# Optimization experiments

Measured on AMD Instinct MI355X. Metric: run time of the kernel, lower is better.

The kernel has to match this reference:

```python
import jax, jax.numpy as jnp
import numpy as np

JITTER = 0.05  # posterior-covariance jitter (constructor arg `jitter`)
TWO_PI = 2.0 * np.pi


def _local_k(x1, x2, ls, std):
    # 1-D RBF kernel: x1 (A,), x2 (B,) -> (A, B)
    d2 = jnp.square(x1[:, None] - x2[None, :])
    return (std * std) * jnp.exp(-0.5 * d2 / (ls * ls))


def setup_inputs() -> dict:
    key = jax.random.key(0)
    ks = jax.random.split(key, 8)
    N, D, M = 3072, 4, 512
    X = jax.random.normal(ks[0], (N, D), dtype=jnp.float32)
    y = jax.random.normal(ks[1], (N, 1), dtype=jnp.float32)
    X_bar = jax.random.normal(ks[2], (M, D), dtype=jnp.float32)
    # learned parameters (moderate positive values so fp32 Choleskys are stable)
    local_gp_ls = 1.0 + 0.1 * jax.random.normal(ks[3], (D,), dtype=jnp.float32)
    local_gp_std = 0.5 + 0.05 * jax.random.normal(ks[4], (D,), dtype=jnp.float32)
    local_gp_noise_std = 0.3 * jnp.ones((D,), dtype=jnp.float32)
    local_ls = 0.3 + 0.5 * jax.random.uniform(ks[5], (M, D), dtype=jnp.float32)
    global_gp_std = jnp.array([0.7], dtype=jnp.float32)
    global_gp_noise_std = jnp.array([0.5], dtype=jnp.float32)
    return {
        "X": X, "y": y, "X_bar": X_bar,
        "local_gp_ls": local_gp_ls, "local_gp_std": local_gp_std,
        "local_gp_noise_std": local_gp_noise_std, "local_ls": local_ls,
        "global_gp_std": global_gp_std, "global_gp_noise_std": global_gp_noise_std,
    }


def reference(X, y, X_bar, local_gp_ls, local_gp_std, local_gp_noise_std,
              local_ls, global_gp_std, global_gp_noise_std):
    # NSGP.nlml() in training mode.
    N, D = X.shape
    M = X_bar.shape[0]
    dtype = X.dtype
    eyeM = jnp.eye(M, dtype=dtype)
    eyeN = jnp.eye(N, dtype=dtype)
    log_lbar = jnp.log(jnp.abs(local_ls))  # (M, D)

    def per_dim(xb, xd, ls, std, noise, loglb):
        # local GP over inducing points for one input dimension
        k = _local_k(xb, xb, ls, std) + (noise * noise) * eyeM  # (M, M)
        c = jnp.linalg.cholesky(k)
        alpha = jax.scipy.linalg.cho_solve((c, True), loglb[:, None])  # (M, 1)
        kstar = _local_k(xd, xb, ls, std)  # (N, M)
        l = jnp.exp(kstar @ alpha)[:, 0]   # (N,) predicted lengthscales
        kss = _local_k(xd, xd, ls, std)    # (N, N)
        v = jax.scipy.linalg.cho_solve((c, True), kstar.T)  # (M, N)
        kpost = kss - kstar @ v + JITTER * eyeN             # posterior cov
        pc = jnp.linalg.cholesky(kpost)
        Bd = jnp.sum(jnp.log(jnp.diagonal(pc)))
        return l, Bd

    # batch the per-dimension local-GP work across the D input dims
    l_dn, B_d = jax.vmap(per_dim, in_axes=(1, 1, 0, 0, 0, 1))(
        X_bar, X, local_gp_ls, local_gp_std, local_gp_noise_std, log_lbar)
    l = l_dn.T  # (N, D)

    # nonstationary global kernel (Gibbs kernel)
    l1 = l[:, None, :]                    # (N, 1, D)
    l2 = l[None, :, :]                    # (1, N, D)
    lsq = l1 * l1 + l2 * l2               # (N, N, D)
    suffix = jnp.prod(jnp.sqrt(2.0 * l1 * l2 / lsq), axis=2)  # (N, N)
    d2 = jnp.square(X[:, None, :] - X[None, :, :])            # (N, N, D)
    gvar = global_gp_std[0] * global_gp_std[0]
    K = gvar * suffix * jnp.exp(-jnp.sum(d2 / lsq, axis=2))
    K = K + (global_gp_noise_std[0] ** 2) * eyeN

    L = jnp.linalg.cholesky(K)
    alpha = jax.scipy.linalg.cho_solve((L, True), y)  # (N, 1)
    log2pi = jnp.log(jnp.asarray(TWO_PI, dtype))
    A = 0.5 * ((y.T @ alpha)[0, 0]
               + jnp.sum(jnp.log(jnp.diagonal(L)))
               + N * log2pi)
    B = jnp.sum(B_d) + 0.5 * (M * D * log2pi)
    return A + B
```

## Files before the change

kernel.cpp:

```cpp
#include <hip/hip_runtime.h>
#include <math.h>

#define N_   3072
#define D_   4
#define M_   512
#define NPAD 3200
#define NB   128
#define PW   32
#define NBLK (NPAD/NB)
#define MBLK (M_/NB)
#define JITTER_ 0.05f
#define CBORD 32768.0f

__global__ __launch_bounds__(256)
void k_potrf_inv(float* Abase, size_t aStride, int lda, int kblk,
                 float* TinvBase, size_t tStride, int doInv,
                 float* logsum, int slotBase, int limit) {
  __shared__ float LT[NB*NB];
  __shared__ float Wp[10*PW*PW];
  __shared__ float Tt[3*PW*PW];
  __shared__ float pivd[NB];
  const int tid = threadIdx.x;
  float* A = Abase + (size_t)blockIdx.z * aStride;
  const int j0 = kblk * NB;

  for (int t = tid; t < NB*NB; t += 256) {
    int r = t & 127, c = t >> 7;
    LT[c*NB + r] = (c <= r) ? A[(size_t)(j0 + r)*lda + (j0 + c)] : 0.f;
  }
  __syncthreads();

  #pragma unroll
  for (int p = 0; p < 4; ++p) {
    const int pc0 = p*PW, pc1 = pc0 + PW;
    for (int j = pc0; j < pc1; ++j) {
      float d = fmaxf(LT[j*NB + j], 1e-30f);
      if (tid == 0) pivd[j] = d;
      float rd = 1.0f / d;
      int w = pc1 - 1 - j;
      for (int t = tid; t < w*NB; t += 256) {
        int c = j + 1 + (t >> 7);
        int i = t & 127;
        if (i >= c)
          LT[c*NB + i] -= LT[j*NB + i] * LT[j*NB + c] * rd;
      }
      __syncthreads();
    }
    for (int t = tid; t < PW*NB; t += 256) {
      int jc = pc0 + (t >> 7);
      int i  = t & 127;
      float dd = pivd[jc];
      if (i > jc)       LT[jc*NB + i] *= rsqrtf(dd);
      else if (i == jc) LT[jc*NB + i] = sqrtf(dd);
    }
    __syncthreads();
    if (pc1 < NB) {
      const int rem = NB - pc1;
      for (int t = tid; t < rem*rem; t += 256) {
        int cc = t / rem, rr = t - cc*rem;
        int c = pc1 + cc, i = pc1 + rr;
        if (i >= c) {
          float s = 0.f;
          #pragma unroll
          for (int jj = 0; jj < PW; ++jj)
            s += LT[(pc0+jj)*NB + i] * LT[(pc0+jj)*NB + c];
          LT[c*NB + i] -= s;
        }
      }
      __syncthreads();
    }
  }

  for (int t = tid; t < NB*NB; t += 256) {
    int r = t & 127, c = t >> 7;
    if (c <= r) A[(size_t)(j0 + r)*lda + (j0 + c)] = LT[c*NB + r];
  }
  {
    float lg = 0.f;
    if (tid < NB) {
      int g = j0 + tid;
      if (g < limit) lg = 0.5f * logf(pivd[tid]);
    }
    for (int o = 32; o; o >>= 1) lg += __shfl_down(lg, o);
    int wv = tid >> 6;
    if ((tid & 63) == 0 && wv < 2)
      logsum[(slotBase + blockIdx.z*32 + kblk)*2 + wv] = lg;
  }

  if (!doInv) return;

  for (int t = tid; t < 4*1024; t += 256) {
    int I = t >> 10, e = t & 1023;
    int r = e >> 5, c = e & 31;
    Wp[(I*(I+1)/2 + I)*1024 + e] = (r == c) ? 1.f : 0.f;
  }
  __syncthreads();
  {
    int wI = tid >> 6;
    int lane = tid & 63;
    float* Rb = &Wp[(wI*(wI+1)/2 + wI)*1024];
    for (int j = 0; j < 32; ++j) {
      float dinv = 1.0f / LT[(wI*32+j)*NB + (wI*32+j)];
      for (int t = lane; t < 1024; t += 64) {
        int i = t >> 5, c = t & 31;
        if (i > j && c <= j)
          Rb[i*32 + c] -= LT[(wI*32+j)*NB + (wI*32+i)] * Rb[j*32 + c] * dinv;
      }
      __syncthreads();
    }
    for (int t = lane; t < 1024; t += 64) {
      int i = t >> 5, c = t & 31;
      if (c <= i) Rb[t] *= 1.0f / LT[(wI*32+i)*NB + (wI*32+i)];
    }
    __syncthreads();
  }
  #pragma unroll
  for (int dist = 1; dist < 4; ++dist) {
    const int nb = 4 - dist;
    for (int t = tid; t < nb*1024; t += 256) {
      int b = t >> 10, e = t & 1023;
      int r = e >> 5, c = e & 31;
      int J = b, I = b + dist;
      float s = 0.f;
      for (int K = J; K < I; ++K) {
        const float* Wkj = &Wp[(K*(K+1)/2 + J)*1024];
        #pragma unroll
        for (int k = 0; k < 32; ++k)
          s += LT[(K*32+k)*NB + (I*32+r)] * Wkj[k*32 + c];
      }
      Tt[b*1024 + e] = s;
    }
    __syncthreads();
    for (int t = tid; t < nb*1024; t += 256) {
      int b = t >> 10, e = t & 1023;
      int r = e >> 5, c = e & 31;
      int J = b, I = b + dist;
      const float* Wii = &Wp[(I*(I+1)/2 + I)*1024];
      float s = 0.f;
      #pragma unroll
      for (int k = 0; k < 32; ++k)
        s += Wii[r*32 + k] * Tt[b*1024 + k*32 + c];
      Wp[(I*(I+1)/2 + J)*1024 + e] = -s;
    }
    __syncthreads();
  }
  {
    float* Tinv = TinvBase + (size_t)blockIdx.z * tStride;
    for (int t = tid; t < NB*32; t += 256) {
      int i = t >> 5, c4 = (t & 31) * 4;
      int I = i >> 5, J = c4 >> 5;
      float4 v;
      if (J <= I) {
        const float* Wij = &Wp[(I*(I+1)/2 + J)*1024 + (i & 31)*32 + (c4 & 31)];
        v = *(const float4*)Wij;
      } else v = make_float4(0.f, 0.f, 0.f, 0.f);
      *(float4*)&Tinv[i*NB + c4] = v;
    }
  }
}

__global__ __launch_bounds__(256)
void k_trsm(float* Abase, size_t aStride, int lda, int kblk,
            const float* TinvBase, size_t tStride) {
  __shared__ float As[32*68];
  __shared__ float Ts[32*132];
  const int tid = threadIdx.x;
  float* A = Abase + (size_t)blockIdx.z * aStride;
  const float* Tinv = TinvBase + (size_t)blockIdx.z * tStride;
  const int k0 = kblk * NB;
  const int row0 = k0 + NB + blockIdx.x * 64;
  const int tx = tid & 15, ty = tid >> 4;
  float acc[4][8];
  #pragma unroll
  for (int i = 0; i < 4; ++i)
    #pragma unroll
    for (int u = 0; u < 8; ++u) acc[i][u] = 0.f;
  for (int ks = 0; ks < NB; ks += 32) {
    for (int t = tid; t < 64*8; t += 256) {
      int r = t >> 3, q = t & 7;
      float4 v = *(const float4*)&A[(size_t)(row0 + r)*lda + k0 + ks + q*4];
      As[(q*4+0)*68 + r] = v.x; As[(q*4+1)*68 + r] = v.y;
      As[(q*4+2)*68 + r] = v.z; As[(q*4+3)*68 + r] = v.w;
    }
    for (int t = tid; t < 128*8; t += 256) {
      int c = t >> 3, q = t & 7;
      float4 v = *(const float4*)&Tinv[c*NB + ks + q*4];
      Ts[(q*4+0)*132 + c] = v.x; Ts[(q*4+1)*132 + c] = v.y;
      Ts[(q*4+2)*132 + c] = v.z; Ts[(q*4+3)*132 + c] = v.w;
    }
    __syncthreads();
    #pragma unroll
    for (int kk = 0; kk < 32; ++kk) {
      float a[4], b[8];
      *(float4*)a      = *(const float4*)&As[kk*68 + ty*4];
      *(float4*)&b[0]  = *(const float4*)&Ts[kk*132 + tx*8];
      *(float4*)&b[4]  = *(const float4*)&Ts[kk*132 + tx*8 + 4];
      #pragma unroll
      for (int i = 0; i < 4; ++i)
        #pragma unroll
        for (int u = 0; u < 8; ++u) acc[i][u] += a[i]*b[u];
    }
    __syncthreads();
  }
  #pragma unroll
  for (int i = 0; i < 4; ++i) {
    int r = row0 + ty*4 + i;
    *(float4*)&A[(size_t)r*lda + k0 + tx*8]     = make_float4(acc[i][0],acc[i][1],acc[i][2],acc[i][3]);
    *(float4*)&A[(size_t)r*lda + k0 + tx*8 + 4] = make_float4(acc[i][4],acc[i][5],acc[i][6],acc[i][7]);
  }
}

__global__ __launch_bounds__(256)
void k_syrk(float* Abase, size_t aStride, int lda, int kblk) {
  if (blockIdx.y > blockIdx.x) return;
  __shared__ float As[32*68];
  __shared__ float Bs[32*68];
  const int tid = threadIdx.x;
  float* A = Abase + (size_t)blockIdx.z * aStride;
  const int k0 = kblk * NB;
  const int row0 = k0 + NB + blockIdx.x * 64;
  const int col0 = k0 + NB + blockIdx.y * 64;
  const int tx = tid & 15, ty = tid >> 4;
  float acc[4][4];
  #pragma unroll
  for (int i=0;i<4;++i) { acc[i][0]=0.f;acc[i][1]=0.f;acc[i][2]=0.f;acc[i][3]=0.f; }
  for (int ks = 0; ks < NB; ks += 32) {
    for (int t = tid; t < 64*8; t += 256) {
      int r = t >> 3, q = t & 7;
      float4 v = *(const float4*)&A[(size_t)(row0 + r)*lda + k0 + ks + q*4];
      As[(q*4+0)*68 + r] = v.x; As[(q*4+1)*68 + r] = v.y;
      As[(q*4+2)*68 + r] = v.z; As[(q*4+3)*68 + r] = v.w;
      float4 w = *(const float4*)&A[(size_t)(col0 + r)*lda + k0 + ks + q*4];
      Bs[(q*4+0)*68 + r] = w.x; Bs[(q*4+1)*68 + r] = w.y;
      Bs[(q*4+2)*68 + r] = w.z; Bs[(q*4+3)*68 + r] = w.w;
    }
    __syncthreads();
    #pragma unroll
    for (int kk = 0; kk < 32; ++kk) {
      float a[4], b[4];
      *(float4*)a = *(const float4*)&As[kk*68 + ty*4];
      *(float4*)b = *(const float4*)&Bs[kk*68 + tx*4];
      #pragma unroll
      for (int i=0;i<4;++i)
        #pragma unroll
        for (int u=0;u<4;++u) acc[i][u] += a[i]*b[u];
    }
    __syncthreads();
  }
  #pragma unroll
  for (int i=0;i<4;++i) {
    size_t off = (size_t)(row0 + ty*4 + i)*lda + col0 + tx*4;
    float4 v = *(const float4*)&A[off];
    v.x -= acc[i][0]; v.y -= acc[i][1]; v.z -= acc[i][2]; v.w -= acc[i][3];
    *(float4*)&A[off] = v;
  }
}

__global__ __launch_bounds__(256)
void k_build_kb(const float* Xbar, const float* lsp, const float* stdp, const float* noisep,
                float* KbBase, size_t kbStride, int dimBase) {
  int z = blockIdx.z, d = dimBase + z;
  float* Kb = KbBase + (size_t)z*kbStride;
  int idx = blockIdx.x*256 + threadIdx.x;
  if (idx >= M_*M_) return;
  int i = idx >> 9, j = idx & 511;
  float ls = lsp[d], sd = stdp[d], nz = noisep[d];
  float df = Xbar[i*D_ + d] - Xbar[j*D_ + d];
  float v = sd*sd*expf(-0.5f*df*df/(ls*ls));
  if (i == j) v += nz*nz;
  Kb[idx] = v;
}

__global__ __launch_bounds__(256)
void k_build_kstar(const float* X, const float* Xbar, const float* lsp, const float* stdp,
                   float* KSBase, size_t ksStride, int dimBase) {
  int z = blockIdx.z, d = dimBase + z;
  float* KS = KSBase + (size_t)z*ksStride;
  int idx = blockIdx.x*256 + threadIdx.x;
  if (idx >= N_*M_) return;
  int i = idx >> 9, j = idx & 511;
  float ls = lsp[d], sd = stdp[d];
  float df = X[i*D_ + d] - Xbar[j*D_ + d];
  KS[idx] = sd*sd*expf(-0.5f*df*df/(ls*ls));
}

__global__ __launch_bounds__(256)
void k_csolve(float* CBase, size_t cStride, const float* KbBase, size_t kbStride,
              const float* TinvKbBase, size_t tkbStride, int J) {
  __shared__ float sm[12672];
  const int tid = threadIdx.x;
  float* C = CBase + (size_t)blockIdx.z*cStride;
  const float* L = KbBase + (size_t)blockIdx.z*kbStride;
  const float* Tinv = TinvKbBase + (size_t)blockIdx.z*tkbStride + (size_t)J*NB*NB;
  const int row0 = blockIdx.x*64;
  const int tx = tid & 15, ty = tid >> 4;
  float* As = sm; float* Ls = sm + 2176;
  float* Xs = sm; float* Ts = sm + 8448;
  float acc[4][8];
  #pragma unroll
  for (int i=0;i<4;++i) {
    const float* p = &C[(size_t)(row0+ty*4+i)*M_ + J*NB + tx*8];
    float4 v0 = *(const float4*)p, v1 = *(const float4*)(p+4);
    acc[i][0]=v0.x; acc[i][1]=v0.y; acc[i][2]=v0.z; acc[i][3]=v0.w;
    acc[i][4]=v1.x; acc[i][5]=v1.y; acc[i][6]=v1.z; acc[i][7]=v1.w;
  }
  for (int P = 0; P < J; ++P) {
    for (int ks = 0; ks < NB; ks += 32) {
      __syncthreads();
      for (int t = tid; t < 64*8; t += 256) {
        int r = t >> 3, q = t & 7;
        float4 v = *(const float4*)&C[(size_t)(row0+r)*M_ + P*NB + ks + q*4];
        As[(q*4+0)*68+r]=v.x; As[(q*4+1)*68+r]=v.y; As[(q*4+2)*68+r]=v.z; As[(q*4+3)*68+r]=v.w;
      }
      for (int t = tid; t < 128*8; t += 256) {
        int c = t >> 3, q = t & 7;
        float4 v = *(const float4*)&L[(size_t)(J*NB+c)*M_ + P*NB + ks + q*4];
        Ls[(q*4+0)*132+c]=v.x; Ls[(q*4+1)*132+c]=v.y; Ls[(q*4+2)*132+c]=v.z; Ls[(q*4+3)*132+c]=v.w;
      }
      __syncthreads();
      #pragma unroll
      for (int kk = 0; kk < 32; ++kk) {
        float a[4], b[8];
        *(float4*)a     = *(const float4*)&As[kk*68 + ty*4];
        *(float4*)&b[0] = *(const float4*)&Ls[kk*132 + tx*8];
        *(float4*)&b[4] = *(const float4*)&Ls[kk*132 + tx*8 + 4];
        #pragma unroll
        for (int i=0;i<4;++i)
          #pragma unroll
          for (int u=0;u<8;++u) acc[i][u] -= a[i]*b[u];
      }
    }
  }
  __syncthreads();
  #pragma unroll
  for (int i=0;i<4;++i)
    #pragma unroll
    for (int u=0;u<8;++u) Xs[(ty*4+i)*132 + tx*8+u] = acc[i][u];
  #pragma unroll
  for (int i=0;i<4;++i)
    #pragma unroll
    for (int u=0;u<8;++u) acc[i][u] = 0.f;
  for (int ms = 0; ms < NB; ms += 32) {
    for (int t = tid; t < 128*8; t += 256) {
      int c = t >> 3, q = t & 7;
      float4 v = *(const float4*)&Tinv[c*NB + ms + q*4];
      Ts[(q*4+0)*132+c]=v.x; Ts[(q*4+1)*132+c]=v.y; Ts[(q*4+2)*132+c]=v.z; Ts[(q*4+3)*132+c]=v.w;
    }
    __syncthreads();
    #pragma unroll
    for (int mm = 0; mm < 32; ++mm) {
      float a[4], b[8];
      a[0]=Xs[(ty*4+0)*132+ms+mm]; a[1]=Xs[(ty*4+1)*132+ms+mm];
      a[2]=Xs[(ty*4+2)*132+ms+mm]; a[3]=Xs[(ty*4+3)*132+ms+mm];
      *(float4*)&b[0] = *(const float4*)&Ts[mm*132 + tx*8];
      *(float4*)&b[4] = *(const float4*)&Ts[mm*132 + tx*8 + 4];
      #pragma unroll
      for (int i=0;i<4;++i)
        #pragma unroll
        for (int u=0;u<8;++u) acc[i][u] += a[i]*b[u];
    }
    __syncthreads();
  }
  #pragma unroll
  for (int i=0;i<4;++i) {
    float* p = &C[(size_t)(row0+ty*4+i)*M_ + J*NB + tx*8];
    *(float4*)p     = make_float4(acc[i][0],acc[i][1],acc[i][2],acc[i][3]);
    *(float4*)(p+4) = make_float4(acc[i][4],acc[i][5],acc[i][6],acc[i][7]);
  }
}

__global__ __launch_bounds__(256)
void k_fwdsub(const float* KbBase, size_t kbStride,
              const float* TkbBase, size_t tkbStride,
              const float* lls, float* wBase, size_t wStride, int dimBase) {
  __shared__ float w[M_];
  __shared__ float tv[NB];
  __shared__ float red[256];
  int z = blockIdx.z, d = dimBase + z;
  const float* L = KbBase + (size_t)z*kbStride;
  const float* Tk = TkbBase + (size_t)z*tkbStride;
  float* wout = wBase + (size_t)z*wStride;
  const int tid = threadIdx.x;
  for (int i = tid; i < M_; i += 256) w[i] = logf(fabsf(lls[i*D_ + d]));
  __syncthreads();
  const int r = tid >> 1, h = tid & 1;
  for (int J = 0; J < 4; ++J) {
    float s = 0.f;
    int half = (J*NB) >> 1;
    for (int k = h*half; k < (h+1)*half; k += 4) {
      float4 lv = *(const float4*)&L[(size_t)(J*NB + r)*M_ + k];
      s += lv.x*w[k] + lv.y*w[k+1] + lv.z*w[k+2] + lv.w*w[k+3];
    }
    red[tid] = s;
    __syncthreads();
    if (h == 0) tv[r] = w[J*NB + r] - red[2*r] - red[2*r+1];
    __syncthreads();
    const float* Ti = Tk + (size_t)J*NB*NB;
    s = 0.f;
    for (int k = h*64; k < h*64 + 64; k += 4) {
      float4 tw = *(const float4*)&Ti[r*NB + k];
      s += tw.x*tv[k] + tw.y*tv[k+1] + tw.z*tv[k+2] + tw.w*tv[k+3];
    }
    red[tid] = s;
    __syncthreads();
    if (h == 0) w[J*NB + r] = red[2*r] + red[2*r+1];
    __syncthreads();
  }
  for (int i = tid; i < M_; i += 256) wout[i] = w[i];
}

__global__ __launch_bounds__(256)
void k_gemv_l(const float* CBase, size_t cStride, const float* wBase, size_t wStride,
              float* lvec, int dimBase) {
  int z = blockIdx.z, d = dimBase + z;
  const float* C = CBase + (size_t)z*cStride;
  const float* w = wBase + (size_t)z*wStride;
  __shared__ float ws[M_];
  for (int i = threadIdx.x; i < M_; i += 256) ws[i] = w[i];
  __syncthreads();
  int wid = threadIdx.x >> 6, lane = threadIdx.x & 63;
  int row = blockIdx.x*4 + wid;
  if (row >= N_) return;
  float s = 0.f;
  const float* cr = &C[(size_t)row*M_];
  for (int k = lane; k < M_; k += 64) s += cr[k]*ws[k];
  for (int o = 32; o; o >>= 1) s += __shfl_down(s, o);
  if (lane == 0) lvec[row*D_ + d] = expf(s);
}

__global__ __launch_bounds__(256)
void k_kpost(const float* X, const float* lsp, const float* stdp,
             const float* CBase, size_t cStride,
             float* Abase, size_t aStride, int dimBase) {
  if (blockIdx.y > blockIdx.x) return;
  __shared__ float As[32*68];
  __shared__ float Bs[32*68];
  int z = blockIdx.z, d = dimBase + z;
  const float* C = CBase + (size_t)z*cStride;
  float* A = Abase + (size_t)z*aStride;
  const int row0 = blockIdx.x*64, col0 = blockIdx.y*64;
  const int tid = threadIdx.x, tx = tid & 15, ty = tid >> 4;
  float acc[4][4];
  #pragma unroll
  for (int i=0;i<4;++i) { acc[i][0]=0.f;acc[i][1]=0.f;acc[i][2]=0.f;acc[i][3]=0.f; }
  if (row0 < N_) {
    for (int ks = 0; ks < M_; ks += 32) {
      for (int t = tid; t < 64*8; t += 256) {
        int r = t >> 3, q = t & 7;
        float4 v = *(const float4*)&C[(size_t)(row0+r)*M_ + ks + q*4];
        As[(q*4+0)*68+r]=v.x; As[(q*4+1)*68+r]=v.y; As[(q*4+2)*68+r]=v.z; As[(q*4+3)*68+r]=v.w;
        float4 w2 = *(const float4*)&C[(size_t)(col0+r)*M_ + ks + q*4];
        Bs[(q*4+0)*68+r]=w2.x; Bs[(q*4+1)*68+r]=w2.y; Bs[(q*4+2)*68+r]=w2.z; Bs[(q*4+3)*68+r]=w2.w;
      }
      __syncthreads();
      #pragma unroll
      for (int kk=0; kk<32; ++kk) {
        float a[4], b[4];
        *(float4*)a = *(const float4*)&As[kk*68 + ty*4];
        *(float4*)b = *(const float4*)&Bs[kk*68 + tx*4];
        #pragma unroll
        for (int i=0;i<4;++i)
          #pragma unroll
          for (int u=0;u<4;++u) acc[i][u] += a[i]*b[u];
      }
      __syncthreads();
    }
  }
  float ls = lsp[d], sd = stdp[d];
  float inv2 = -0.5f/(ls*ls), s2 = sd*sd;
  #pragma unroll
  for (int i=0;i<4;++i) {
    int gi = row0 + ty*4 + i;
    float xi = (gi < N_) ? X[gi*D_ + d] : 0.f;
    #pragma unroll
    for (int u=0;u<4;++u) {
      int gj = col0 + tx*4 + u;
      float v;
      if (gi < N_ && gj < N_) {
        float df = xi - X[gj*D_ + d];
        v = s2*expf(inv2*df*df) - acc[i][u];
        if (gi == gj) v += JITTER_;
      } else {
        v = (gi == gj) ? 1.f : 0.f;
      }
      A[(size_t)gi*NPAD + gj] = v;
    }
  }
}

__global__ __launch_bounds__(256)
void k_kfinal(const float* X, const float* lvec, const float* y,
              const float* gstd, const float* gnoise, float* A) {
  int idx = blockIdx.x*256 + threadIdx.x;
  if (idx >= NPAD*NPAD) return;
  int gi = idx / NPAD, gj = idx - (idx/NPAD)*NPAD;
  float v;
  if (gi < N_ && gj < N_) {
    float gv = gstd[0]*gstd[0];
    float prod = 1.f, s = 0.f;
    #pragma unroll
    for (int d = 0; d < D_; ++d) {
      float l1 = lvec[gi*D_ + d], l2 = lvec[gj*D_ + d];
      float lsq = l1*l1 + l2*l2;
      prod *= 2.f*l1*l2/lsq;
      float df = X[gi*D_ + d] - X[gj*D_ + d];
      s += df*df/lsq;
    }
    v = gv * sqrtf(prod) * expf(-s);
    if (gi == gj) v += gnoise[0]*gnoise[0];
  } else if (gi == N_ && gj < N_) v = y[gj];
  else if (gj == N_ && gi < N_) v = y[gi];
  else if (gi == N_ && gj == N_) v = CBORD;
  else v = (gi == gj) ? 1.f : 0.f;
  A[idx] = v;
}

__global__ void k_finalize(const float* A, const float* logsum, float* out) {
  if (threadIdx.x != 0 || blockIdx.x != 0) return;
  float sumB = 0.f;
  for (int z = 0; z < 4; ++z)
    for (int k = 0; k < NBLK; ++k) {
      int slot = z*32 + k;
      sumB += logsum[slot*2] + logsum[slot*2+1];
    }
  float sumL = 0.f;
  for (int k = 0; k < NBLK; ++k) {
    int slot = 128 + k;
    sumL += logsum[slot*2] + logsum[slot*2+1];
  }
  float lb = A[(size_t)N_*NPAD + N_];
  float yKy = CBORD - lb*lb;
  const float LOG2PI = 1.8378770664093453f;
  float Aterm = 0.5f*(yKy + sumL + (float)N_*LOG2PI);
  float Bterm = sumB + 0.5f*(float)(M_*D_)*LOG2PI;
  out[0] = Aterm + Bterm;
}

extern "C" void kernel_launch(void* const* d_in, const int* in_sizes, int n_in,
                              void* d_out, int out_size, void* d_ws, size_t ws_size,
                              hipStream_t stream) {
  const float* X    = (const float*)d_in[0];
  const float* y    = (const float*)d_in[1];
  const float* Xbar = (const float*)d_in[2];
  const float* lgls = (const float*)d_in[3];
  const float* lgstd= (const float*)d_in[4];
  const float* lgnz = (const float*)d_in[5];
  const float* lls  = (const float*)d_in[6];
  const float* gstd = (const float*)d_in[7];
  const float* gnz  = (const float*)d_in[8];
  float* out = (float*)d_out;

  const size_t A_SZ   = (size_t)NPAD*NPAD;
  const size_t KS_SZ  = (size_t)N_*M_;
  const size_t KB_SZ  = (size_t)M_*M_;
  const size_t TKB_SZ = (size_t)4*NB*NB;
  const size_t TBG_SZ = (size_t)NB*NB;
  const size_t W_SZ   = (size_t)M_;
  const size_t LV_SZ  = (size_t)N_*D_;
  const size_t LOG_SZ = 1024;

  size_t need2 = (5*A_SZ + 4*(KS_SZ + KB_SZ + TKB_SZ + W_SZ) + 5*TBG_SZ
                  + LV_SZ + LOG_SZ + 1024);
  size_t per1  = A_SZ + KS_SZ + KB_SZ + TKB_SZ + TBG_SZ + W_SZ;
  size_t need1 = 4*per1 + LV_SZ + LOG_SZ + 256;

  if (ws_size >= need2 * sizeof(float)) {
    float* p = (float*)d_ws;
    float* A    = p; p += 5*A_SZ;
    float* KS   = p; p += 4*KS_SZ;
    float* Kb   = p; p += 4*KB_SZ;
    float* Tkb  = p; p += 4*TKB_SZ;
    float* Tbig = p; p += 5*TBG_SZ;
    float* wv   = p; p += 4*W_SZ;
    float* lv   = p; p += LV_SZ;
    float* lgs  = p; p += LOG_SZ;

    k_build_kb<<<dim3((M_*M_+255)/256,1,4),256,0,stream>>>(Xbar,lgls,lgstd,lgnz,Kb,KB_SZ,0);
    for (int k = 0; k < MBLK; ++k) {
      k_potrf_inv<<<dim3(1,1,4),256,0,stream>>>(Kb,KB_SZ,M_,k,Tkb+(size_t)k*NB*NB,TKB_SZ,1,lgs,192,0);
      if (k < MBLK-1) {
        int nt = (MBLK-1-k)*2;
        k_trsm<<<dim3(nt,1,4),256,0,stream>>>(Kb,KB_SZ,M_,k,Tkb+(size_t)k*NB*NB,TKB_SZ);
        k_syrk<<<dim3(nt,nt,4),256,0,stream>>>(Kb,KB_SZ,M_,k);
      }
    }
    k_fwdsub<<<dim3(1,1,4),256,0,stream>>>(Kb,KB_SZ,Tkb,TKB_SZ,lls,wv,W_SZ,0);
    k_build_kstar<<<dim3((N_*M_+255)/256,1,4),256,0,stream>>>(X,Xbar,lgls,lgstd,KS,KS_SZ,0);
    for (int J = 0; J < MBLK; ++J)
      k_csolve<<<dim3(N_/64,1,4),256,0,stream>>>(KS,KS_SZ,Kb,KB_SZ,Tkb,TKB_SZ,J);
    k_gemv_l<<<dim3(N_/4,1,4),256,0,stream>>>(KS,KS_SZ,wv,W_SZ,lv,0);
    k_kpost<<<dim3(NPAD/64,NPAD/64,4),256,0,stream>>>(X,lgls,lgstd,KS,KS_SZ,A,A_SZ,0);
    k_kfinal<<<dim3((NPAD*NPAD+255)/256,1,1),256,0,stream>>>(X,lv,y,gstd,gnz,A+4*A_SZ);
    for (int k = 0; k < NBLK; ++k) {
      k_potrf_inv<<<dim3(1,1,5),256,0,stream>>>(A,A_SZ,NPAD,k,Tbig,TBG_SZ,(k<NBLK-1)?1:0,lgs,0,N_);
      if (k < NBLK-1) {
        int nt = (NBLK-1-k)*2;
        k_trsm<<<dim3(nt,1,5),256,0,stream>>>(A,A_SZ,NPAD,k,Tbig,TBG_SZ);
        k_syrk<<<dim3(nt,nt,5),256,0,stream>>>(A,A_SZ,NPAD,k);
      }
    }
    k_finalize<<<1,64,0,stream>>>(A+4*A_SZ,lgs,out);
    return;
  }

  bool batched = ws_size >= need1 * sizeof(float);
  int nz = batched ? 4 : 1;

  float* p = (float*)d_ws;
  float* A    = p; p += (size_t)nz*A_SZ;
  float* KS   = p; p += (size_t)nz*KS_SZ;
  float* Kb   = p; p += (size_t)nz*KB_SZ;
  float* Tkb  = p; p += (size_t)nz*TKB_SZ;
  float* Tbig = p; p += (size_t)nz*TBG_SZ;
  float* wv   = p; p += (size_t)nz*W_SZ;
  float* lv   = p; p += LV_SZ;
  float* lgs  = p; p += LOG_SZ;

  int npass = batched ? 1 : 4;
  for (int pass = 0; pass < npass; ++pass) {
    int dimBase  = batched ? 0 : pass;
    int slotBase = batched ? 0 : pass*32;

    k_build_kb<<<dim3((M_*M_+255)/256,1,nz),256,0,stream>>>(Xbar,lgls,lgstd,lgnz,Kb,KB_SZ,dimBase);
    for (int k = 0; k < MBLK; ++k) {
      k_potrf_inv<<<dim3(1,1,nz),256,0,stream>>>(Kb,KB_SZ,M_,k,Tkb+(size_t)k*NB*NB,TKB_SZ,1,lgs,192+slotBase,0);
      if (k < MBLK-1) {
        int nt = (MBLK-1-k)*2;
        k_trsm<<<dim3(nt,1,nz),256,0,stream>>>(Kb,KB_SZ,M_,k,Tkb+(size_t)k*NB*NB,TKB_SZ);
        k_syrk<<<dim3(nt,nt,nz),256,0,stream>>>(Kb,KB_SZ,M_,k);
      }
    }
    k_fwdsub<<<dim3(1,1,nz),256,0,stream>>>(Kb,KB_SZ,Tkb,TKB_SZ,lls,wv,W_SZ,dimBase);
    k_build_kstar<<<dim3((N_*M_+255)/256,1,nz),256,0,stream>>>(X,Xbar,lgls,lgstd,KS,KS_SZ,dimBase);
    for (int J = 0; J < MBLK; ++J)
      k_csolve<<<dim3(N_/64,1,nz),256,0,stream>>>(KS,KS_SZ,Kb,KB_SZ,Tkb,TKB_SZ,J);
    k_gemv_l<<<dim3(N_/4,1,nz),256,0,stream>>>(KS,KS_SZ,wv,W_SZ,lv,dimBase);
    k_kpost<<<dim3(NPAD/64,NPAD/64,nz),256,0,stream>>>(X,lgls,lgstd,KS,KS_SZ,A,A_SZ,dimBase);
    for (int k = 0; k < NBLK; ++k) {
      k_potrf_inv<<<dim3(1,1,nz),256,0,stream>>>(A,A_SZ,NPAD,k,Tbig,TBG_SZ,(k<NBLK-1)?1:0,lgs,slotBase,N_);
      if (k < NBLK-1) {
        int nt = (NBLK-1-k)*2;
        k_trsm<<<dim3(nt,1,nz),256,0,stream>>>(A,A_SZ,NPAD,k,Tbig,TBG_SZ);
        k_syrk<<<dim3(nt,nt,nz),256,0,stream>>>(A,A_SZ,NPAD,k);
      }
    }
  }

  k_kfinal<<<dim3((NPAD*NPAD+255)/256,1,1),256,0,stream>>>(X,lv,y,gstd,gnz,A);
  for (int k = 0; k < NBLK; ++k) {
    k_potrf_inv<<<dim3(1,1,1),256,0,stream>>>(A,A_SZ,NPAD,k,Tbig,TBG_SZ,(k<NBLK-1)?1:0,lgs,128,N_);
    if (k < NBLK-1) {
      int nt = (NBLK-1-k)*2;
      k_trsm<<<dim3(nt,1,1),256,0,stream>>>(A,A_SZ,NPAD,k,Tbig,TBG_SZ);
      k_syrk<<<dim3(nt,nt,1),256,0,stream>>>(A,A_SZ,NPAD,k);
    }
  }
  k_finalize<<<1,64,0,stream>>>(A,lgs,out);
}
```

Measured before the change: 8.406 ms.

## Fuse next-panel potrf into the trailing syrk kernel (lookahead Cholesky)

Replaces the separate potrf and syrk launches with one k_step kernel per block step. Block 0 first applies the pending rank-128 update to the next diagonal block itself (presub), then factors and inverts it, while the other blocks apply the trailing SYRK update to the rest of the matrix. This overlaps the serial single-block factorization with the parallel trailing update and removes one launch per step. It also uses 512-thread blocks, padded shared-memory strides, and 4x4 register tiling for the in-block update. The cost is heavy shared-memory use that limits each CU to one block (launch bounds 512,1), and correctness depends on the triangular tile indexing skipping the diagonal tiles that block 0 handles.

```diff
diff --git a/kernel.cpp b/kernel.cpp
--- a/kernel.cpp
+++ b/kernel.cpp
@@ -11,152 +11,281 @@
 #define MBLK (M_/NB)
 #define JITTER_ 0.05f
 #define CBORD 32768.0f
-
-__global__ __launch_bounds__(256)
-void k_potrf_inv(float* Abase, size_t aStride, int lda, int kblk,
-                 float* TinvBase, size_t tStride, int doInv,
-                 float* logsum, int slotBase, int limit) {
-  __shared__ float LT[NB*NB];
-  __shared__ float Wp[10*PW*PW];
-  __shared__ float Tt[3*PW*PW];
-  __shared__ float pivd[NB];
+#define LTS  132
+
+__device__ void syrk64(float* A, int lda, int gr0, int gc0, int k0, int valid,
+                       float* As, float* Bs, int lt) {
+  const int tx = lt & 15, ty = lt >> 4;
+  float acc[4][4];
+  #pragma unroll
+  for (int i=0;i<4;++i){acc[i][0]=0.f;acc[i][1]=0.f;acc[i][2]=0.f;acc[i][3]=0.f;}
+  for (int ks = 0; ks < NB; ks += 32) {
+    __syncthreads();
+    if (valid) {
+      for (int t = lt; t < 64*8; t += 256) {
+        int rr = t >> 3, qq = t & 7;
+        float4 v = *(const float4*)&A[(size_t)(gr0+rr)*lda + k0 + ks + qq*4];
+        As[(qq*4+0)*68+rr]=v.x; As[(qq*4+1)*68+rr]=v.y;
+        As[(qq*4+2)*68+rr]=v.z; As[(qq*4+3)*68+rr]=v.w;
+        float4 w = *(const float4*)&A[(size_t)(gc0+rr)*lda + k0 + ks + qq*4];
+        Bs[(qq*4+0)*68+rr]=w.x; Bs[(qq*4+1)*68+rr]=w.y;
+        Bs[(qq*4+2)*68+rr]=w.z; Bs[(qq*4+3)*68+rr]=w.w;
+      }
+    }
+    __syncthreads();
+    if (valid) {
+      #pragma unroll
+      for (int kk = 0; kk < 32; ++kk) {
+        float a[4], b[4];
+        *(float4*)a = *(const float4*)&As[kk*68 + ty*4];
+        *(float4*)b = *(const float4*)&Bs[kk*68 + tx*4];
+        #pragma unroll
+        for (int i=0;i<4;++i)
+          #pragma unroll
+          for (int u=0;u<4;++u) acc[i][u] += a[i]*b[u];
+      }
+    }
+  }
+  if (valid) {
+    #pragma unroll
+    for (int i=0;i<4;++i) {
+      size_t off = (size_t)(gr0 + ty*4 + i)*lda + gc0 + tx*4;
+      float4 v = *(const float4*)&A[off];
+      v.x -= acc[i][0]; v.y -= acc[i][1]; v.z -= acc[i][2]; v.w -= acc[i][3];
+      *(float4*)&A[off] = v;
+    }
+  }
+}
+
+__device__ void presub64(const float* A, int lda, int j0, int p0, int sr, int sc,
+                         int valid, float* As, float* Bs, float* LT_, int lt) {
+  const int tx = lt & 15, ty = lt >> 4;
+  float acc[4][4];
+  #pragma unroll
+  for (int i=0;i<4;++i){acc[i][0]=0.f;acc[i][1]=0.f;acc[i][2]=0.f;acc[i][3]=0.f;}
+  for (int ks = 0; ks < NB; ks += 32) {
+    __syncthreads();
+    if (valid) {
+      for (int t = lt; t < 64*8; t += 256) {
+        int rr = t >> 3, qq = t & 7;
+        float4 v = *(const float4*)&A[(size_t)(j0+sr*64+rr)*lda + p0 + ks + qq*4];
+        As[(qq*4+0)*68+rr]=v.x; As[(qq*4+1)*68+rr]=v.y;
+        As[(qq*4+2)*68+rr]=v.z; As[(qq*4+3)*68+rr]=v.w;
+        float4 w = *(const float4*)&A[(size_t)(j0+sc*64+rr)*lda + p0 + ks + qq*4];
+        Bs[(qq*4+0)*68+rr]=w.x; Bs[(qq*4+1)*68+rr]=w.y;
+        Bs[(qq*4+2)*68+rr]=w.z; Bs[(qq*4+3)*68+rr]=w.w;
+      }
+    }
+    __syncthreads();
+    if (valid) {
+      #pragma unroll
+      for (int kk = 0; kk < 32; ++kk) {
+        float a[4], b[4];
+        *(float4*)a = *(const float4*)&As[kk*68 + ty*4];
+        *(float4*)b = *(const float4*)&Bs[kk*68 + tx*4];
+        #pragma unroll
+        for (int i=0;i<4;++i)
+          #pragma unroll
+          for (int u=0;u<4;++u) acc[i][u] += a[i]*b[u];
+      }
+    }
+  }
+  if (valid) {
+    #pragma unroll
+    for (int i=0;i<4;++i)
+      #pragma unroll
+      for (int u=0;u<4;++u) {
+        int rr = sr*64 + ty*4 + i, cc = sc*64 + tx*4 + u;
+        if (cc <= rr) LT_[cc*LTS + rr] -= acc[i][u];
+      }
+  }
+}
+
+__device__ void potrf_duty(float* A, int lda, int b, int presub, int doInv,
+                           float* Tinv, float* logsum, int slot, int limit,
+                           float* LT_, float* SM_, float* pivd_) {
   const int tid = threadIdx.x;
-  float* A = Abase + (size_t)blockIdx.z * aStride;
-  const int j0 = kblk * NB;
-
-  for (int t = tid; t < NB*NB; t += 256) {
-    int r = t & 127, c = t >> 7;
-    LT[c*NB + r] = (c <= r) ? A[(size_t)(j0 + r)*lda + (j0 + c)] : 0.f;
+  const int j0 = b * NB;
+  for (int t = tid; t < NB*NB; t += 512) {
+    int r = t >> 7, c = t & 127;
+    float v = 0.f;
+    if (c <= r) v = A[(size_t)(j0+r)*lda + (j0+c)];
+    LT_[c*LTS + r] = v;
+  }
+  if (presub) {
+    int half = tid >> 8, lt = tid & 255;
+    float* As = SM_ + half*4352; float* Bs = As + 2176;
+    const int p0 = j0 - NB;
+    presub64(A, lda, j0, p0, half, 0, 1, As, Bs, LT_, lt);
+    presub64(A, lda, j0, p0, 1, 1, half==0 ? 1 : 0, As, Bs, LT_, lt);
   }
   __syncthreads();
-
   #pragma unroll
   for (int p = 0; p < 4; ++p) {
     const int pc0 = p*PW, pc1 = pc0 + PW;
     for (int j = pc0; j < pc1; ++j) {
-      float d = fmaxf(LT[j*NB + j], 1e-30f);
-      if (tid == 0) pivd[j] = d;
-      float rd = 1.0f / d;
-      int w = pc1 - 1 - j;
-      for (int t = tid; t < w*NB; t += 256) {
+      float dd = fmaxf(LT_[j*LTS + j], 1e-30f);
+      if (tid == 0) pivd_[j] = dd;
+      float rd = 1.0f / dd;
+      int wn = pc1 - 1 - j;
+      for (int t = tid; t < wn*NB; t += 512) {
         int c = j + 1 + (t >> 7);
         int i = t & 127;
-        if (i >= c)
-          LT[c*NB + i] -= LT[j*NB + i] * LT[j*NB + c] * rd;
+        if (i >= c) LT_[c*LTS + i] -= LT_[j*LTS + i] * LT_[j*LTS + c] * rd;
       }
       __syncthreads();
     }
-    for (int t = tid; t < PW*NB; t += 256) {
+    for (int t = tid; t < PW*NB; t += 512) {
       int jc = pc0 + (t >> 7);
       int i  = t & 127;
-      float dd = pivd[jc];
-      if (i > jc)       LT[jc*NB + i] *= rsqrtf(dd);
-      else if (i == jc) LT[jc*NB + i] = sqrtf(dd);
+      float dd = pivd_[jc];
+      if (i > jc)       LT_[jc*LTS + i] *= rsqrtf(dd);
+      else if (i == jc) LT_[jc*LTS + i] = sqrtf(dd);
     }
     __syncthreads();
     if (pc1 < NB) {
-      const int rem = NB - pc1;
-      for (int t = tid; t < rem*rem; t += 256) {
-        int cc = t / rem, rr = t - cc*rem;
-        int c = pc1 + cc, i = pc1 + rr;
-        if (i >= c) {
-          float s = 0.f;
+      const int rem = NB - pc1, g4 = rem >> 2;
+      for (int t = tid; t < g4*g4; t += 512) {
+        int tr = t / g4, tc = t - tr*g4;
+        if (tc > tr) continue;
+        int i0 = pc1 + tr*4, c0 = pc1 + tc*4;
+        float acc2[4][4];
+        #pragma unroll
+        for (int i=0;i<4;++i){acc2[i][0]=0.f;acc2[i][1]=0.f;acc2[i][2]=0.f;acc2[i][3]=0.f;}
+        #pragma unroll
+        for (int jj = 0; jj < PW; ++jj) {
+          float av[4], bv[4];
+          *(float4*)av = *(const float4*)&LT_[(pc0+jj)*LTS + i0];
+          *(float4*)bv = *(const float4*)&LT_[(pc0+jj)*LTS + c0];
           #pragma unroll
-          for (int jj = 0; jj < PW; ++jj)
-            s += LT[(pc0+jj)*NB + i] * LT[(pc0+jj)*NB + c];
-          LT[c*NB + i] -= s;
+          for (int i=0;i<4;++i)
+            #pragma unroll
+            for (int u=0;u<4;++u) acc2[i][u] += av[i]*bv[u];
         }
+        #pragma unroll
+        for (int i=0;i<4;++i)
+          #pragma unroll
+          for (int u=0;u<4;++u) {
+            int rr = i0+i, cc = c0+u;
+            if (cc <= rr) LT_[cc*LTS + rr] -= acc2[i][u];
+          }
       }
       __syncthreads();
     }
   }
-
-  for (int t = tid; t < NB*NB; t += 256) {
-    int r = t & 127, c = t >> 7;
-    if (c <= r) A[(size_t)(j0 + r)*lda + (j0 + c)] = LT[c*NB + r];
+  for (int t = tid; t < NB*NB; t += 512) {
+    int r = t >> 7, c = t & 127;
+    if (c <= r) A[(size_t)(j0+r)*lda + (j0+c)] = LT_[c*LTS + r];
   }
   {
     float lg = 0.f;
     if (tid < NB) {
       int g = j0 + tid;
-      if (g < limit) lg = 0.5f * logf(pivd[tid]);
+      if (g < limit) lg = 0.5f * logf(pivd_[tid]);
     }
     for (int o = 32; o; o >>= 1) lg += __shfl_down(lg, o);
     int wv = tid >> 6;
-    if ((tid & 63) == 0 && wv < 2)
-      logsum[(slotBase + blockIdx.z*32 + kblk)*2 + wv] = lg;
-  }
-
+    if ((tid & 63) == 0 && wv < 2) logsum[slot*2 + wv] = lg;
+  }
   if (!doInv) return;
-
-  for (int t = tid; t < 4*1024; t += 256) {
+  float* Wp = SM_;
+  float* Tt = SM_ + 10240;
+  for (int t = tid; t < 4*1024; t += 512) {
     int I = t >> 10, e = t & 1023;
     int r = e >> 5, c = e & 31;
     Wp[(I*(I+1)/2 + I)*1024 + e] = (r == c) ? 1.f : 0.f;
   }
   __syncthreads();
   {
-    int wI = tid >> 6;
-    int lane = tid & 63;
+    int wI = tid >> 7;
+    int lane = tid & 127;
     float* Rb = &Wp[(wI*(wI+1)/2 + wI)*1024];
     for (int j = 0; j < 32; ++j) {
-      float dinv = 1.0f / LT[(wI*32+j)*NB + (wI*32+j)];
-      for (int t = lane; t < 1024; t += 64) {
+      float dinv = 1.0f / LT_[(wI*32+j)*LTS + (wI*32+j)];
+      for (int t = lane; t < 1024; t += 128) {
         int i = t >> 5, c = t & 31;
         if (i > j && c <= j)
-          Rb[i*32 + c] -= LT[(wI*32+j)*NB + (wI*32+i)] * Rb[j*32 + c] * dinv;
+          Rb[i*32 + c] -= LT_[(wI*32+j)*LTS + (wI*32+i)] * Rb[j*32 + c] * dinv;
       }
       __syncthreads();
     }
-    for (int t = lane; t < 1024; t += 64) {
+    for (int t = lane; t < 1024; t += 128) {
       int i = t >> 5, c = t & 31;
-      if (c <= i) Rb[t] *= 1.0f / LT[(wI*32+i)*NB + (wI*32+i)];
+      if (c <= i) Rb[i*32 + c] *= 1.0f / LT_[(wI*32+i)*LTS + (wI*32+i)];
     }
     __syncthreads();
   }
   #pragma unroll
   for (int dist = 1; dist < 4; ++dist) {
     const int nb = 4 - dist;
-    for (int t = tid; t < nb*1024; t += 256) {
-      int b = t >> 10, e = t & 1023;
+    for (int t = tid; t < nb*1024; t += 512) {
+      int bb = t >> 10, e = t & 1023;
       int r = e >> 5, c = e & 31;
-      int J = b, I = b + dist;
+      int J = bb, I = bb + dist;
       float s = 0.f;
       for (int K = J; K < I; ++K) {
         const float* Wkj = &Wp[(K*(K+1)/2 + J)*1024];
         #pragma unroll
         for (int k = 0; k < 32; ++k)
-          s += LT[(K*32+k)*NB + (I*32+r)] * Wkj[k*32 + c];
-      }
-      Tt[b*1024 + e] = s;
-    }
-    __syncthreads();
-    for (int t = tid; t < nb*1024; t += 256) {
-      int b = t >> 10, e = t & 1023;
+          s += LT_[(K*32+k)*LTS + (I*32+r)] * Wkj[k*32 + c];
+      }
+      Tt[bb*1024 + e] = s;
+    }
+    __syncthreads();
+    for (int t = tid; t < nb*1024; t += 512) {
+      int bb = t >> 10, e = t & 1023;
       int r = e >> 5, c = e & 31;
-      int J = b, I = b + dist;
+      int J = bb, I = bb + dist;
       const float* Wii = &Wp[(I*(I+1)/2 + I)*1024];
       float s = 0.f;
       #pragma unroll
       for (int k = 0; k < 32; ++k)
-        s += Wii[r*32 + k] * Tt[b*1024 + k*32 + c];
+        s += Wii[r*32 + k] * Tt[bb*1024 + k*32 + c];
       Wp[(I*(I+1)/2 + J)*1024 + e] = -s;
     }
     __syncthreads();
   }
-  {
-    float* Tinv = TinvBase + (size_t)blockIdx.z * tStride;
-    for (int t = tid; t < NB*32; t += 256) {
-      int i = t >> 5, c4 = (t & 31) * 4;
-      int I = i >> 5, J = c4 >> 5;
-      float4 v;
-      if (J <= I) {
-        const float* Wij = &Wp[(I*(I+1)/2 + J)*1024 + (i & 31)*32 + (c4 & 31)];
-        v = *(const float4*)Wij;
-      } else v = make_float4(0.f, 0.f, 0.f, 0.f);
-      *(float4*)&Tinv[i*NB + c4] = v;
-    }
-  }
+  for (int t = tid; t < NB*32; t += 512) {
+    int i = t >> 5, c4 = (t & 31) * 4;
+    int I = i >> 5, J = c4 >> 5;
+    float4 v;
+    if (J <= I) {
+      const float* Wij = &Wp[(I*(I+1)/2 + J)*1024 + (i & 31)*32 + (c4 & 31)];
+      v = *(const float4*)Wij;
+    } else v = make_float4(0.f, 0.f, 0.f, 0.f);
+    *(float4*)&Tinv[i*NB + c4] = v;
+  }
+}
+
+__global__ __launch_bounds__(512, 1)
+void k_step(float* Abase, size_t aStride, int lda, int bpot, int presub, int doInv,
+            float* TinvBase, size_t tStrideZ, size_t tStrideK,
+            float* logsum, int slotBase, int limit,
+            int R0, int q, int k0) {
+  __shared__ __align__(16) float LT[128*LTS];
+  __shared__ __align__(16) float SM[13312];
+  __shared__ float pivd[NB];
+  const int z = blockIdx.z;
+  float* A = Abase + (size_t)z*aStride;
+
+  if (blockIdx.x == 0) {
+    potrf_duty(A, lda, bpot, presub, doInv,
+               TinvBase + (size_t)z*tStrideZ + (size_t)bpot*tStrideK,
+               logsum, slotBase + z*32 + bpot, limit, LT, SM, pivd);
+    return;
+  }
+  const int tid = threadIdx.x;
+  int half = tid >> 8, lt = tid & 255;
+  int tileIdx = (blockIdx.x - 1)*2 + half;
+  int ntiles = q*(q+1)/2 - 3;
+  int valid = (tileIdx < ntiles) ? 1 : 0;
+  int idxp = valid ? tileIdx + 3 : 3;
+  int r = (int)((sqrtf(8.f*(float)idxp + 1.f) - 1.f)*0.5f);
+  while ((r+1)*(r+2)/2 <= idxp) ++r;
+  while (r*(r+1)/2 > idxp) --r;
+  int c = idxp - r*(r+1)/2;
+  syrk64(A, lda, (R0+r)*64, (R0+c)*64, k0, valid,
+         SM + half*4352, SM + half*4352 + 2176, lt);
 }
 
 __global__ __launch_bounds__(256)
@@ -207,52 +336,6 @@
     int r = row0 + ty*4 + i;
     *(float4*)&A[(size_t)r*lda + k0 + tx*8]     = make_float4(acc[i][0],acc[i][1],acc[i][2],acc[i][3]);
     *(float4*)&A[(size_t)r*lda + k0 + tx*8 + 4] = make_float4(acc[i][4],acc[i][5],acc[i][6],acc[i][7]);
-  }
-}
-
-__global__ __launch_bounds__(256)
-void k_syrk(float* Abase, size_t aStride, int lda, int kblk) {
-  if (blockIdx.y > blockIdx.x) return;
-  __shared__ float As[32*68];
-  __shared__ float Bs[32*68];
-  const int tid = threadIdx.x;
-  float* A = Abase + (size_t)blockIdx.z * aStride;
-  const int k0 = kblk * NB;
-  const int row0 = k0 + NB + blockIdx.x * 64;
-  const int col0 = k0 + NB + blockIdx.y * 64;
-  const int tx = tid & 15, ty = tid >> 4;
-  float acc[4][4];
-  #pragma unroll
-  for (int i=0;i<4;++i) { acc[i][0]=0.f;acc[i][1]=0.f;acc[i][2]=0.f;acc[i][3]=0.f; }
-  for (int ks = 0; ks < NB; ks += 32) {
-    for (int t = tid; t < 64*8; t += 256) {
-      int r = t >> 3, q = t & 7;
-      float4 v = *(const float4*)&A[(size_t)(row0 + r)*lda + k0 + ks + q*4];
-      As[(q*4+0)*68 + r] = v.x; As[(q*4+1)*68 + r] = v.y;
-      As[(q*4+2)*68 + r] = v.z; As[(q*4+3)*68 + r] = v.w;
-      float4 w = *(const float4*)&A[(size_t)(col0 + r)*lda + k0 + ks + q*4];
-      Bs[(q*4+0)*68 + r] = w.x; Bs[(q*4+1)*68 + r] = w.y;
-      Bs[(q*4+2)*68 + r] = w.z; Bs[(q*4+3)*68 + r] = w.w;
-    }
-    __syncthreads();
-    #pragma unroll
-    for (int kk = 0; kk < 32; ++kk) {
-      float a[4], b[4];
-      *(float4*)a = *(const float4*)&As[kk*68 + ty*4];
-      *(float4*)b = *(const float4*)&Bs[kk*68 + tx*4];
-      #pragma unroll
-      for (int i=0;i<4;++i)
-        #pragma unroll
-        for (int u=0;u<4;++u) acc[i][u] += a[i]*b[u];
-    }
-    __syncthreads();
-  }
-  #pragma unroll
-  for (int i=0;i<4;++i) {
-    size_t off = (size_t)(row0 + ty*4 + i)*lda + col0 + tx*4;
-    float4 v = *(const float4*)&A[off];
-    v.x -= acc[i][0]; v.y -= acc[i][1]; v.z -= acc[i][2]; v.w -= acc[i][3];
-    *(float4*)&A[off] = v;
   }
 }
 
@@ -536,6 +619,24 @@
   out[0] = Aterm + Bterm;
 }
 
+static void run_chain(float* A, size_t aS, int lda, int nblk,
+                      float* Tinv, size_t tz, size_t tk, int invAll,
+                      float* lgs, int slotBase, int limit, int nz,
+                      hipStream_t stream) {
+  int doInv0 = (invAll || nblk > 1) ? 1 : 0;
+  k_step<<<dim3(1,1,nz),512,0,stream>>>(A,aS,lda, 0,0,doInv0, Tinv,tz,tk,
+                                        lgs,slotBase,limit, 0,0,0);
+  for (int k = 0; k < nblk-1; ++k) {
+    int m = nblk-1-k;
+    k_trsm<<<dim3(2*m,1,nz),256,0,stream>>>(A,aS,lda,k, Tinv + (size_t)k*tk, tz);
+    int q2 = 2*m, ntiles = q2*(q2+1)/2 - 3;
+    int nbx = 1 + (ntiles+1)/2;
+    int doInv = (invAll || (k+1 < nblk-1)) ? 1 : 0;
+    k_step<<<dim3(nbx,1,nz),512,0,stream>>>(A,aS,lda, k+1,1,doInv, Tinv,tz,tk,
+                                            lgs,slotBase,limit, (k+1)*2, q2, k*NB);
+  }
+}
+
 extern "C" void kernel_launch(void* const* d_in, const int* in_sizes, int n_in,
                               void* d_out, int out_size, void* d_ws, size_t ws_size,
                               hipStream_t stream) {
@@ -576,14 +677,7 @@
     float* lgs  = p; p += LOG_SZ;
 
     k_build_kb<<<dim3((M_*M_+255)/256,1,4),256,0,stream>>>(Xbar,lgls,lgstd,lgnz,Kb,KB_SZ,0);
-    for (int k = 0; k < MBLK; ++k) {
-      k_potrf_inv<<<dim3(1,1,4),256,0,stream>>>(Kb,KB_SZ,M_,k,Tkb+(size_t)k*NB*NB,TKB_SZ,1,lgs,192,0);
-      if (k < MBLK-1) {
-        int nt = (MBLK-1-k)*2;
-        k_trsm<<<dim3(nt,1,4),256,0,stream>>>(Kb,KB_SZ,M_,k,Tkb+(size_t)k*NB*NB,TKB_SZ);
-        k_syrk<<<dim3(nt,nt,4),256,0,stream>>>(Kb,KB_SZ,M_,k);
-      }
-    }
+    run_chain(Kb, KB_SZ, M_, MBLK, Tkb, TKB_SZ, (size_t)NB*NB, 1, lgs, 192, 0, 4, stream);
     k_fwdsub<<<dim3(1,1,4),256,0,stream>>>(Kb,KB_SZ,Tkb,TKB_SZ,lls,wv,W_SZ,0);
     k_build_kstar<<<dim3((N_*M_+255)/256,1,4),256,0,stream>>>(X,Xbar,lgls,lgstd,KS,KS_SZ,0);
     for (int J = 0; J < MBLK; ++J)
@@ -591,21 +685,13 @@
     k_gemv_l<<<dim3(N_/4,1,4),256,0,stream>>>(KS,KS_SZ,wv,W_SZ,lv,0);
     k_kpost<<<dim3(NPAD/64,NPAD/64,4),256,0,stream>>>(X,lgls,lgstd,KS,KS_SZ,A,A_SZ,0);
     k_kfinal<<<dim3((NPAD*NPAD+255)/256,1,1),256,0,stream>>>(X,lv,y,gstd,gnz,A+4*A_SZ);
-    for (int k = 0; k < NBLK; ++k) {
-      k_potrf_inv<<<dim3(1,1,5),256,0,stream>>>(A,A_SZ,NPAD,k,Tbig,TBG_SZ,(k<NBLK-1)?1:0,lgs,0,N_);
-      if (k < NBLK-1) {
-        int nt = (NBLK-1-k)*2;
-        k_trsm<<<dim3(nt,1,5),256,0,stream>>>(A,A_SZ,NPAD,k,Tbig,TBG_SZ);
-        k_syrk<<<dim3(nt,nt,5),256,0,stream>>>(A,A_SZ,NPAD,k);
-      }
-    }
+    run_chain(A, A_SZ, NPAD, NBLK, Tbig, TBG_SZ, 0, 0, lgs, 0, N_, 5, stream);
     k_finalize<<<1,64,0,stream>>>(A+4*A_SZ,lgs,out);
     return;
   }
 
   bool batched = ws_size >= need1 * sizeof(float);
   int nz = batched ? 4 : 1;
-
   float* p = (float*)d_ws;
   float* A    = p; p += (size_t)nz*A_SZ;
   float* KS   = p; p += (size_t)nz*KS_SZ;
@@ -620,40 +706,17 @@
   for (int pass = 0; pass < npass; ++pass) {
     int dimBase  = batched ? 0 : pass;
     int slotBase = batched ? 0 : pass*32;
-
     k_build_kb<<<dim3((M_*M_+255)/256,1,nz),256,0,stream>>>(Xbar,lgls,lgstd,lgnz,Kb,KB_SZ,dimBase);
-    for (int k = 0; k < MBLK; ++k) {
-      k_potrf_inv<<<dim3(1,1,nz),256,0,stream>>>(Kb,KB_SZ,M_,k,Tkb+(size_t)k*NB*NB,TKB_SZ,1,lgs,192+slotBase,0);
-      if (k < MBLK-1) {
-        int nt = (MBLK-1-k)*2;
-        k_trsm<<<dim3(nt,1,nz),256,0,stream>>>(Kb,KB_SZ,M_,k,Tkb+(size_t)k*NB*NB,TKB_SZ);
-        k_syrk<<<dim3(nt,nt,nz),256,0,stream>>>(Kb,KB_SZ,M_,k);
-      }
-    }
+    run_chain(Kb, KB_SZ, M_, MBLK, Tkb, TKB_SZ, (size_t)NB*NB, 1, lgs, 192+slotBase, 0, nz, stream);
     k_fwdsub<<<dim3(1,1,nz),256,0,stream>>>(Kb,KB_SZ,Tkb,TKB_SZ,lls,wv,W_SZ,dimBase);
     k_build_kstar<<<dim3((N_*M_+255)/256,1,nz),256,0,stream>>>(X,Xbar,lgls,lgstd,KS,KS_SZ,dimBase);
     for (int J = 0; J < MBLK; ++J)
       k_csolve<<<dim3(N_/64,1,nz),256,0,stream>>>(KS,KS_SZ,Kb,KB_SZ,Tkb,TKB_SZ,J);
     k_gemv_l<<<dim3(N_/4,1,nz),256,0,stream>>>(KS,KS_SZ,wv,W_SZ,lv,dimBase);
     k_kpost<<<dim3(NPAD/64,NPAD/64,nz),256,0,stream>>>(X,lgls,lgstd,KS,KS_SZ,A,A_SZ,dimBase);
-    for (int k = 0; k < NBLK; ++k) {
-      k_potrf_inv<<<dim3(1,1,nz),256,0,stream>>>(A,A_SZ,NPAD,k,Tbig,TBG_SZ,(k<NBLK-1)?1:0,lgs,slotBase,N_);
-      if (k < NBLK-1) {
-        int nt = (NBLK-1-k)*2;
-        k_trsm<<<dim3(nt,1,nz),256,0,stream>>>(A,A_SZ,NPAD,k,Tbig,TBG_SZ);
-        k_syrk<<<dim3(nt,nt,nz),256,0,stream>>>(A,A_SZ,NPAD,k);
-      }
-    }
-  }
-
+    run_chain(A, A_SZ, NPAD, NBLK, Tbig, TBG_SZ, 0, 0, lgs, slotBase, N_, nz, stream);
+  }
   k_kfinal<<<dim3((NPAD*NPAD+255)/256,1,1),256,0,stream>>>(X,lv,y,gstd,gnz,A);
-  for (int k = 0; k < NBLK; ++k) {
-    k_potrf_inv<<<dim3(1,1,1),256,0,stream>>>(A,A_SZ,NPAD,k,Tbig,TBG_SZ,(k<NBLK-1)?1:0,lgs,128,N_);
-    if (k < NBLK-1) {
-      int nt = (NBLK-1-k)*2;
-      k_trsm<<<dim3(nt,1,1),256,0,stream>>>(A,A_SZ,NPAD,k,Tbig,TBG_SZ);
-      k_syrk<<<dim3(nt,nt,1),256,0,stream>>>(A,A_SZ,NPAD,k);
-    }
-  }
+  run_chain(A, A_SZ, NPAD, NBLK, Tbig, TBG_SZ, 0, 0, lgs, 128, N_, 1, stream);
   k_finalize<<<1,64,0,stream>>>(A,lgs,out);
 }
```

Result: faster. 8.000 ms (-4.8%).
